# Optimization experiments

Measured on AMD Instinct MI355X. Metric: run time of the kernel, lower is better.

The kernel has to match this reference:

```python
import jax, jax.numpy as jnp
import numpy as np

MAX_DISP = 48


def setup_inputs() -> dict:
    key = jax.random.key(0)
    k1, k2 = jax.random.split(key)
    n, c, h, w = 2, 32, 128, 256
    l_fmap = jax.random.normal(k1, (n, c, h, w), dtype=jnp.float32)
    r_fmap = jax.random.normal(k2, (n, c, h, w), dtype=jnp.float32)
    return {"l_fmap": l_fmap, "r_fmap": r_fmap}


def reference(l_fmap, r_fmap):
    # Cost volume: out[n,c,d,h,x] = l[n,c,h,x] - r[n,c,h,x-d] for x >= d, else 1.0
    n, c, h, w = l_fmap.shape
    d = jnp.arange(MAX_DISP)                      # [D]
    shift = jnp.arange(w)[None, :] - d[:, None]   # [D, W] source column in r
    valid = shift >= 0                            # [D, W]
    r_g = r_fmap[:, :, :, jnp.clip(shift, 0)]     # [n, c, h, D, W] gather of shifted right fmap
    one = jnp.asarray(1.0, l_fmap.dtype)
    cost = jnp.where(valid[None, None, None], l_fmap[:, :, :, None, :] - r_g, one)
    return jnp.transpose(cost, (0, 1, 3, 2, 4))   # [n, c, D, h, W]
```

## Files before the change

kernel.cpp:

```cpp
#include <hip/hip_runtime.h>

#define MAX_DISP 48


constexpr int W  = 256;
constexpr int H  = 128;
constexpr int D  = MAX_DISP;
constexpr int HW = H * W;

typedef float vf4 __attribute__((ext_vector_type(4)));

template <int WAVE>
__device__ __forceinline__ void run_passes(const vf4* __restrict__ rs4,
                                           int lane, int xq, vf4 lv,
                                           float* __restrict__ obase)
{
    vf4 wlo = rs4[max(lane - 1, 0)];
    vf4 whi = rs4[lane];

    #pragma unroll
    for (int k = 0; k < 12; ++k) {
        const int d = WAVE + 4 * k;

        float rv0, rv1, rv2, rv3;
        if constexpr (WAVE == 0) { rv0 = whi.x; rv1 = whi.y; rv2 = whi.z; rv3 = whi.w; }
        else if constexpr (WAVE == 1) { rv0 = wlo.w; rv1 = whi.x; rv2 = whi.y; rv3 = whi.z; }
        else if constexpr (WAVE == 2) { rv0 = wlo.z; rv1 = wlo.w; rv2 = whi.x; rv3 = whi.y; }
        else                          { rv0 = wlo.y; rv1 = wlo.z; rv2 = wlo.w; rv3 = whi.x; }

        vf4 o;
        o.x = (xq + 0 >= d) ? lv.x - rv0 : 1.0f;
        o.y = (xq + 1 >= d) ? lv.y - rv1 : 1.0f;
        o.z = (xq + 2 >= d) ? lv.z - rv2 : 1.0f;
        o.w = (xq + 3 >= d) ? lv.w - rv3 : 1.0f;

        __builtin_nontemporal_store(
            o, reinterpret_cast<vf4*>(obase + (size_t)d * HW + xq));

        if (k < 11) {
            whi = wlo;
            wlo = rs4[max(lane - k - 2, 0)];
        }
    }
}

__global__ __launch_bounds__(256) void cost_volume_kernel(
    const float* __restrict__ l,
    const float* __restrict__ r,
    float* __restrict__ out)
{
    const int row = blockIdx.x;
    const int h   = row % H;
    const int nc  = row / H;

    __shared__ float rs[W];

    const int t    = threadIdx.x;
    const int wave = t >> 6;
    const int lane = t & 63;
    const int xq   = lane << 2;

    const float* __restrict__ lrow = l + (size_t)row * W;
    const float* __restrict__ rrow = r + (size_t)row * W;

    rs[t] = rrow[t];

    const vf4 lv = *reinterpret_cast<const vf4*>(lrow + xq);
    float* obase = out + (size_t)nc * D * HW + (size_t)h * W;

    __syncthreads();

    const vf4* rs4 = reinterpret_cast<const vf4*>(rs);
    switch (wave) {
        case 0: run_passes<0>(rs4, lane, xq, lv, obase); break;
        case 1: run_passes<1>(rs4, lane, xq, lv, obase); break;
        case 2: run_passes<2>(rs4, lane, xq, lv, obase); break;
        default: run_passes<3>(rs4, lane, xq, lv, obase); break;
    }
}

extern "C" void kernel_launch(void* const* d_in, const int* in_sizes, int n_in,
                              void* d_out, int out_size, void* d_ws, size_t ws_size,
                              hipStream_t stream)
{
    const float* l = (const float*)d_in[0];
    const float* r = (const float*)d_in[1];
    float* out = (float*)d_out;

    const int nRows = 2 * 32 * H;
    cost_volume_kernel<<<nRows, 256, 0, stream>>>(l, r, out);
}
```

Baseline: 69.00 us.

## Process eight rows per block to batch stores and cut block count

```diff
diff --git a/kernel.cpp b/kernel.cpp
--- a/kernel.cpp
+++ b/kernel.cpp
@@ -7,39 +7,51 @@
 constexpr int H  = 128;
 constexpr int D  = MAX_DISP;
 constexpr int HW = H * W;
+constexpr int HG = 8;
 
 typedef float vf4 __attribute__((ext_vector_type(4)));
 
 template <int WAVE>
 __device__ __forceinline__ void run_passes(const vf4* __restrict__ rs4,
-                                           int lane, int xq, vf4 lv,
+                                           int lane, int xq,
+                                           const vf4* __restrict__ lv,
                                            float* __restrict__ obase)
 {
-    vf4 wlo = rs4[max(lane - 1, 0)];
-    vf4 whi = rs4[lane];
+    vf4 wlo[HG], whi[HG];
+    #pragma unroll
+    for (int rr = 0; rr < HG; ++rr) {
+        wlo[rr] = rs4[rr * 64 + max(lane - 1, 0)];
+        whi[rr] = rs4[rr * 64 + lane];
+    }
 
-    #pragma unroll
     for (int k = 0; k < 12; ++k) {
         const int d = WAVE + 4 * k;
+        float* __restrict__ od = obase + (size_t)d * HW + xq;
 
-        float rv0, rv1, rv2, rv3;
-        if constexpr (WAVE == 0) { rv0 = whi.x; rv1 = whi.y; rv2 = whi.z; rv3 = whi.w; }
-        else if constexpr (WAVE == 1) { rv0 = wlo.w; rv1 = whi.x; rv2 = whi.y; rv3 = whi.z; }
-        else if constexpr (WAVE == 2) { rv0 = wlo.z; rv1 = wlo.w; rv2 = whi.x; rv3 = whi.y; }
-        else                          { rv0 = wlo.y; rv1 = wlo.z; rv2 = wlo.w; rv3 = whi.x; }
+        #pragma unroll
+        for (int rr = 0; rr < HG; ++rr) {
+            float rv0, rv1, rv2, rv3;
+            if constexpr (WAVE == 0) { rv0 = whi[rr].x; rv1 = whi[rr].y; rv2 = whi[rr].z; rv3 = whi[rr].w; }
+            else if constexpr (WAVE == 1) { rv0 = wlo[rr].w; rv1 = whi[rr].x; rv2 = whi[rr].y; rv3 = whi[rr].z; }
+            else if constexpr (WAVE == 2) { rv0 = wlo[rr].z; rv1 = wlo[rr].w; rv2 = whi[rr].x; rv3 = whi[rr].y; }
+            else                          { rv0 = wlo[rr].y; rv1 = wlo[rr].z; rv2 = wlo[rr].w; rv3 = whi[rr].x; }
 
-        vf4 o;
-        o.x = (xq + 0 >= d) ? lv.x - rv0 : 1.0f;
-        o.y = (xq + 1 >= d) ? lv.y - rv1 : 1.0f;
-        o.z = (xq + 2 >= d) ? lv.z - rv2 : 1.0f;
-        o.w = (xq + 3 >= d) ? lv.w - rv3 : 1.0f;
+            vf4 o;
+            o.x = (xq + 0 >= d) ? lv[rr].x - rv0 : 1.0f;
+            o.y = (xq + 1 >= d) ? lv[rr].y - rv1 : 1.0f;
+            o.z = (xq + 2 >= d) ? lv[rr].z - rv2 : 1.0f;
+            o.w = (xq + 3 >= d) ? lv[rr].w - rv3 : 1.0f;
 
-        __builtin_nontemporal_store(
-            o, reinterpret_cast<vf4*>(obase + (size_t)d * HW + xq));
+            __builtin_nontemporal_store(o, reinterpret_cast<vf4*>(od + rr * W));
+        }
 
         if (k < 11) {
-            whi = wlo;
-            wlo = rs4[max(lane - k - 2, 0)];
+            const int src = max(lane - k - 2, 0);
+            #pragma unroll
+            for (int rr = 0; rr < HG; ++rr) {
+                whi[rr] = wlo[rr];
+                wlo[rr] = rs4[rr * 64 + src];
+            }
         }
     }
 }
@@ -49,24 +61,31 @@
     const float* __restrict__ r,
     float* __restrict__ out)
 {
-    const int row = blockIdx.x;
-    const int h   = row % H;
-    const int nc  = row / H;
+    const int b  = blockIdx.x;
+    const int hg = b & (H / HG - 1);
+    const int nc = b >> 4;
+    const int h0 = hg * HG;
 
-    __shared__ float rs[W];
+    __shared__ float rs[HG * W];
 
     const int t    = threadIdx.x;
     const int wave = t >> 6;
     const int lane = t & 63;
     const int xq   = lane << 2;
 
-    const float* __restrict__ lrow = l + (size_t)row * W;
-    const float* __restrict__ rrow = r + (size_t)row * W;
+    const vf4* __restrict__ rsrc =
+        reinterpret_cast<const vf4*>(r + (size_t)(nc * H + h0) * W);
+    vf4* rdst = reinterpret_cast<vf4*>(rs);
+    rdst[t]       = rsrc[t];
+    rdst[t + 256] = rsrc[t + 256];
 
-    rs[t] = rrow[t];
+    vf4 lv[HG];
+    #pragma unroll
+    for (int rr = 0; rr < HG; ++rr)
+        lv[rr] = *reinterpret_cast<const vf4*>(
+            l + (size_t)(nc * H + h0 + rr) * W + xq);
 
-    const vf4 lv = *reinterpret_cast<const vf4*>(lrow + xq);
-    float* obase = out + (size_t)nc * D * HW + (size_t)h * W;
+    float* obase = out + (size_t)nc * D * HW + (size_t)h0 * W;
 
     __syncthreads();
 
@@ -87,6 +106,6 @@
     const float* r = (const float*)d_in[1];
     float* out = (float*)d_out;
 
-    const int nRows = 2 * 32 * H;
-    cost_volume_kernel<<<nRows, 256, 0, stream>>>(l, r, out);
+    const int nBlk = 64 * (H / HG);
+    cost_volume_kernel<<<nBlk, 256, 0, stream>>>(l, r, out);
 }
```

Result: slower. 79.90 us (+15.8%).

## Assign one row per wave with all disparities, four rows per block

Applied to the files above, without the earlier changes.

```diff
diff --git a/kernel.cpp b/kernel.cpp
--- a/kernel.cpp
+++ b/kernel.cpp
@@ -7,26 +7,48 @@
 constexpr int H  = 128;
 constexpr int D  = MAX_DISP;
 constexpr int HW = H * W;
+constexpr int RPB = 4;
 
 typedef float vf4 __attribute__((ext_vector_type(4)));
 
-template <int WAVE>
-__device__ __forceinline__ void run_passes(const vf4* __restrict__ rs4,
-                                           int lane, int xq, vf4 lv,
-                                           float* __restrict__ obase)
+__global__ __launch_bounds__(256) void cost_volume_kernel(
+    const float* __restrict__ l,
+    const float* __restrict__ r,
+    float* __restrict__ out)
 {
-    vf4 wlo = rs4[max(lane - 1, 0)];
-    vf4 whi = rs4[lane];
+    const int b    = blockIdx.x;
+    const int hq   = b & (H / RPB - 1);
+    const int nc   = b >> 5;
+    const int t    = threadIdx.x;
+    const int wave = t >> 6;
+    const int lane = t & 63;
+    const int xq   = lane << 2;
+    const int h    = hq * RPB + wave;
+    const int row  = nc * H + h;
+
+    __shared__ float rs[RPB * W];
+
+    vf4* rs4w = reinterpret_cast<vf4*>(rs) + wave * 64;
+    rs4w[lane] = reinterpret_cast<const vf4*>(r + (size_t)row * W)[lane];
+
+    const vf4 lv = reinterpret_cast<const vf4*>(l + (size_t)row * W)[lane];
+
+    float* obase = out + (size_t)nc * D * HW + (size_t)h * W + xq;
+
+    __syncthreads();
+
+    vf4 whi = rs4w[lane];
+    vf4 wlo = rs4w[max(lane - 1, 0)];
 
     #pragma unroll
-    for (int k = 0; k < 12; ++k) {
-        const int d = WAVE + 4 * k;
+    for (int d = 0; d < D; ++d) {
+        const int ph = d & 3;
 
         float rv0, rv1, rv2, rv3;
-        if constexpr (WAVE == 0) { rv0 = whi.x; rv1 = whi.y; rv2 = whi.z; rv3 = whi.w; }
-        else if constexpr (WAVE == 1) { rv0 = wlo.w; rv1 = whi.x; rv2 = whi.y; rv3 = whi.z; }
-        else if constexpr (WAVE == 2) { rv0 = wlo.z; rv1 = wlo.w; rv2 = whi.x; rv3 = whi.y; }
-        else                          { rv0 = wlo.y; rv1 = wlo.z; rv2 = wlo.w; rv3 = whi.x; }
+        if (ph == 0)      { rv0 = whi.x; rv1 = whi.y; rv2 = whi.z; rv3 = whi.w; }
+        else if (ph == 1) { rv0 = wlo.w; rv1 = whi.x; rv2 = whi.y; rv3 = whi.z; }
+        else if (ph == 2) { rv0 = wlo.z; rv1 = wlo.w; rv2 = whi.x; rv3 = whi.y; }
+        else              { rv0 = wlo.y; rv1 = wlo.z; rv2 = wlo.w; rv3 = whi.x; }
 
         vf4 o;
         o.x = (xq + 0 >= d) ? lv.x - rv0 : 1.0f;
@@ -35,47 +57,12 @@
         o.w = (xq + 3 >= d) ? lv.w - rv3 : 1.0f;
 
         __builtin_nontemporal_store(
-            o, reinterpret_cast<vf4*>(obase + (size_t)d * HW + xq));
+            o, reinterpret_cast<vf4*>(obase + (size_t)d * HW));
 
-        if (k < 11) {
+        if (ph == 3 && d < D - 1) {
             whi = wlo;
-            wlo = rs4[max(lane - k - 2, 0)];
+            wlo = rs4w[max(lane - (d >> 2) - 2, 0)];
         }
-    }
-}
-
-__global__ __launch_bounds__(256) void cost_volume_kernel(
-    const float* __restrict__ l,
-    const float* __restrict__ r,
-    float* __restrict__ out)
-{
-    const int row = blockIdx.x;
-    const int h   = row % H;
-    const int nc  = row / H;
-
-    __shared__ float rs[W];
-
-    const int t    = threadIdx.x;
-    const int wave = t >> 6;
-    const int lane = t & 63;
-    const int xq   = lane << 2;
-
-    const float* __restrict__ lrow = l + (size_t)row * W;
-    const float* __restrict__ rrow = r + (size_t)row * W;
-
-    rs[t] = rrow[t];
-
-    const vf4 lv = *reinterpret_cast<const vf4*>(lrow + xq);
-    float* obase = out + (size_t)nc * D * HW + (size_t)h * W;
-
-    __syncthreads();
-
-    const vf4* rs4 = reinterpret_cast<const vf4*>(rs);
-    switch (wave) {
-        case 0: run_passes<0>(rs4, lane, xq, lv, obase); break;
-        case 1: run_passes<1>(rs4, lane, xq, lv, obase); break;
-        case 2: run_passes<2>(rs4, lane, xq, lv, obase); break;
-        default: run_passes<3>(rs4, lane, xq, lv, obase); break;
     }
 }
 
@@ -87,6 +74,6 @@
     const float* r = (const float*)d_in[1];
     float* out = (float*)d_out;
 
-    const int nRows = 2 * 32 * H;
-    cost_volume_kernel<<<nRows, 256, 0, stream>>>(l, r, out);
+    const int nBlk = 64 * (H / RPB);
+    cost_volume_kernel<<<nBlk, 256, 0, stream>>>(l, r, out);
 }
```

Measured after the change: 77.45 us. 12.3% more time.
